# Kernel optimization log

Hardware: AMD Instinct MI355X
Metric: run time of the kernel (lower is better)

Reference implementation:

```python
import jax, jax.numpy as jnp
import numpy as np

VIEW_NUM = 360
CHAN_NUM = 512
BATCH = 2
IMG = 512


def setup_inputs() -> dict:
    key = jax.random.key(0)
    x = jax.random.normal(key, (BATCH, 1, IMG, IMG), dtype=jnp.float32)
    return {"x": x}


def _bilinear_sample_zeros(img, ix, iy):
    """Bilinear sample img (B,1,H,W) at pixel coords ix, iy (H,W), zeros padding.
    Matches F.grid_sample(mode='bilinear', padding_mode='zeros', align_corners=False)."""
    H, W = img.shape[-2], img.shape[-1]
    x0 = jnp.floor(ix)
    y0 = jnp.floor(iy)
    x1 = x0 + 1.0
    y1 = y0 + 1.0
    wx1 = ix - x0
    wx0 = 1.0 - wx1
    wy1 = iy - y0
    wy0 = 1.0 - wy1

    def gather(yy, xx):
        valid = (xx >= 0) & (xx <= W - 1) & (yy >= 0) & (yy <= H - 1)
        xi = jnp.clip(xx, 0, W - 1).astype(jnp.int32)
        yi = jnp.clip(yy, 0, H - 1).astype(jnp.int32)
        # fancy-index over spatial dims -> (B,1,H,W)
        return img[:, :, yi, xi] * valid.astype(img.dtype)

    return (gather(y0, x0) * (wy0 * wx0)
            + gather(y0, x1) * (wy0 * wx1)
            + gather(y1, x0) * (wy1 * wx0)
            + gather(y1, x1) * (wy1 * wx1))


def _fp(x):
    B, C, H, W = x.shape
    # affine_grid base coords, align_corners=False: (2i+1)/N - 1
    bx = (2.0 * jnp.arange(W, dtype=x.dtype) + 1.0) / W - 1.0
    by = (2.0 * jnp.arange(H, dtype=x.dtype) + 1.0) / H - 1.0
    X = bx[None, :]  # (1,W)
    Y = by[:, None]  # (H,1)
    i = jnp.arange(VIEW_NUM, dtype=x.dtype)
    angles = -jnp.pi * (i + 1.0) / VIEW_NUM - jnp.pi
    cosv = jnp.cos(angles)
    sinv = jnp.sin(angles)

    def per_view(carry, cs):
        c, s = cs
        # theta = [[c,-s,0],[s,c,0]]; grid = base @ theta^T
        gx = c * X - s * Y  # (H,W) normalized sample x
        gy = s * X + c * Y  # (H,W) normalized sample y
        # unnormalize (align_corners=False)
        ix = ((gx + 1.0) * W - 1.0) * 0.5
        iy = ((gy + 1.0) * H - 1.0) * 0.5
        samp = _bilinear_sample_zeros(x, ix, iy)  # (B,1,H,W)
        return carry, jnp.sum(samp, axis=2)  # sum over height -> (B,1,W)

    _, cols = jax.lax.scan(per_view, 0, (cosv, sinv))  # (V,B,1,W)
    sino = jnp.transpose(cols, (1, 2, 3, 0)) * 0.5  # (B,1,chanNum,viewNum)
    return sino


def reference(x):
    return _fp(x)
```

## Files before the change

### kernel.cpp

```cpp
#include <hip/hip_runtime.h>

typedef __fp16 h2 __attribute__((ext_vector_type(2)));

constexpr int VIEWS = 360;
constexpr int IMGSZ = 512;
constexpr int WCHUNK = 64;
constexpr int KH = 64;
constexpr int PITCH = 101;
constexpr int MAXNY = 94;
constexpr int LDSDW = PITCH * MAXNY;
constexpr int PW = 712;
constexpr int PH = 704;
constexpr int PAD = 96;
constexpr int NT = 512;

__global__ __launch_bounds__(256) void pad_kernel(const float* __restrict__ x,
                                                  unsigned* __restrict__ padq) {
    constexpr int PW4 = PW / 4;
    constexpr int total = PH * PW4;
    int idx = blockIdx.x * 256 + threadIdx.x;
    if (idx >= total) return;
    int py = idx / PW4;
    int px4 = idx - py * PW4;
    int gx = px4 * 4 - PAD;
    int gy = py - PAD;
    const float* img0 = x;
    const float* img1 = x + (size_t)IMGSZ * IMGSZ;
    float4 a = make_float4(0.f, 0.f, 0.f, 0.f);
    float4 bq = a;
    if ((unsigned)gy < (unsigned)IMGSZ && (unsigned)gx < (unsigned)IMGSZ) {
        size_t off = (size_t)gy * IMGSZ + gx;
        a  = *(const float4*)(img0 + off);
        bq = *(const float4*)(img1 + off);
    }
    uint4 d;
    d.x = __builtin_bit_cast(unsigned, __builtin_amdgcn_cvt_pkrtz(a.x, bq.x));
    d.y = __builtin_bit_cast(unsigned, __builtin_amdgcn_cvt_pkrtz(a.y, bq.y));
    d.z = __builtin_bit_cast(unsigned, __builtin_amdgcn_cvt_pkrtz(a.z, bq.z));
    d.w = __builtin_bit_cast(unsigned, __builtin_amdgcn_cvt_pkrtz(a.w, bq.w));
    *(uint4*)&padq[(size_t)idx * 4] = d;
}

__global__ __launch_bounds__(NT, 8) void fp_kernel(const unsigned* __restrict__ padq,
                                                   float* __restrict__ out) {
    __shared__ __align__(16) unsigned tileU[LDSDW];

    int blk = blockIdx.x;
    int wc = blk & 7;
    int v = blk >> 3;

    int tid = threadIdx.x;
    int lane = tid & 63;
    int p = tid >> 6;
    int w = wc * WCHUNK + lane;

    double ang = -3.14159265358979323846 * (double)(v + 1) / (double)VIEWS
                 - 3.14159265358979323846;
    float c = (float)cos(ang);
    float s = (float)sin(ang);

    float xw = (float)w + 0.5f - 256.0f;
    float cxw = fmaf(c, xw, 255.5f);
    float sxw = fmaf(s, xw, 255.5f);

    float lo = -1e30f, hi = 1e30f;
    {
        float coef = -s, base = cxw;
        if (fabsf(coef) > 1e-6f) {
            float a = (-1.0f - base) / coef;
            float bq = (512.0f - base) / coef;
            lo = fmaxf(lo, fminf(a, bq));
            hi = fminf(hi, fmaxf(a, bq));
        } else if (!(base > -1.0f && base < 512.0f)) {
            lo = 1e30f; hi = -1e30f;
        }
    }
    {
        float coef = c, base = sxw;
        if (fabsf(coef) > 1e-6f) {
            float a = (-1.0f - base) / coef;
            float bq = (512.0f - base) / coef;
            lo = fmaxf(lo, fminf(a, bq));
            hi = fminf(hi, fmaxf(a, bq));
        } else if (!(base > -1.0f && base < 512.0f)) {
            lo = 1e30f; hi = -1e30f;
        }
    }
    float h0f = fminf(fmaxf(floorf(lo + 255.5f) - 1.0f, 0.0f), 512.0f);
    float h1f = fminf(fmaxf(ceilf(hi + 255.5f) + 1.0f, -1.0f), 511.0f);
    int h0 = (int)h0f;
    int h1 = (int)h1f;

    int bh0 = h0, bh1 = h1;
    #pragma unroll
    for (int m = 1; m < 64; m <<= 1) {
        bh0 = min(bh0, __shfl_xor(bh0, m, 64));
        bh1 = max(bh1, __shfl_xor(bh1, m, 64));
    }

    float xa = (float)(wc * WCHUNK) + 0.5f - 256.0f;
    float xb = xa + 63.0f;

    float acc0 = 0.0f, acc1 = 0.0f;
    float step8x = -8.0f * s;
    float step8y = 8.0f * c;

    for (int hc = bh0; hc <= bh1; hc += KH) {
        int hend = min(hc + KH - 1, bh1);

        float ha = (float)hc - 255.5f;
        float hb = (float)hend - 255.5f;
        float ix00 = c * xa - s * ha, ix01 = c * xa - s * hb;
        float ix10 = c * xb - s * ha, ix11 = c * xb - s * hb;
        float iy00 = s * xa + c * ha, iy01 = s * xa + c * hb;
        float iy10 = s * xb + c * ha, iy11 = s * xb + c * hb;
        float ixmn = fminf(fminf(ix00, ix01), fminf(ix10, ix11)) + 255.5f;
        float iymn = fminf(fminf(iy00, iy01), fminf(iy10, iy11)) + 255.5f;
        float iymx = fmaxf(fmaxf(iy00, iy01), fmaxf(iy10, iy11)) + 255.5f;
        int x_lo = (int)floorf(ixmn) - 1;
        int x_lo4 = x_lo & ~3;
        int y_lo = (int)floorf(iymn) - 1;
        int NY = min((int)floorf(iymx) + 3 - y_lo, MAXNY);
        int total4 = NY * 25;
        int nit = (total4 + NT - 1) >> 9;

        __syncthreads();

        {
            const unsigned* pb = padq + (y_lo + PAD) * PW + (x_lo4 + PAD);
            for (int k = 0; k < nit; ++k) {
                int ic = min((k << 9) + tid, total4 - 1);
                int ry = ic / 25;
                uint4 val = *(const uint4*)(pb + 4 * ic + (PW - 100) * ry);
                int d = (ic << 2) + ry;
                tileU[d]     = val.x;
                tileU[d + 1] = val.y;
                tileU[d + 2] = val.z;
                tileU[d + 3] = val.w;
            }
        }
        __syncthreads();

        float hh0 = (float)(hc + p) - 255.5f;
        float ixr = fmaf(-s, hh0, cxw) - (float)x_lo4;
        float iyr = fmaf(c, hh0, sxw) - (float)y_lo;
        h2 accp0 = (h2)0.0f;
        h2 accp1 = (h2)0.0f;
        int parity = 0;
        #pragma unroll 8
        for (int h = hc + p; h <= hend; h += 8) {
            float tx = truncf(ixr);
            float ty = truncf(iyr);
            float wx1 = ixr - tx;
            float wy1 = iyr - ty;
            h2 wxs = __builtin_amdgcn_cvt_pkrtz(wx1, wx1);
            h2 wys = __builtin_amdgcn_cvt_pkrtz(wy1, wy1);
            unsigned a = (unsigned)fmaf(ty, 404.0f, tx * 4.0f);
            const unsigned* pt = (const unsigned*)((const char*)tileU + a);
            h2 t00 = __builtin_bit_cast(h2, pt[0]);
            h2 t01 = __builtin_bit_cast(h2, pt[1]);
            h2 t10 = __builtin_bit_cast(h2, pt[PITCH]);
            h2 t11 = __builtin_bit_cast(h2, pt[PITCH + 1]);
            h2 r0 = t00 + (t01 - t00) * wxs;
            h2 r1 = t10 + (t11 - t10) * wxs;
            h2 contrib = r0 + (r1 - r0) * wys;
            if (parity) accp1 += contrib; else accp0 += contrib;
            parity ^= 1;
            ixr += step8x;
            iyr += step8y;
        }
        acc0 += (float)accp0.x + (float)accp1.x;
        acc1 += (float)accp0.y + (float)accp1.y;
    }

    __syncthreads();
    tileU[(p << 6) + lane] = __float_as_uint(acc0);
    tileU[512 + (p << 6) + lane] = __float_as_uint(acc1);
    __syncthreads();
    if (p < 2) {
        const unsigned* base = tileU + (p << 9);
        float r = 0.0f;
        #pragma unroll
        for (int q = 0; q < 8; ++q) r += __uint_as_float(base[(q << 6) + lane]);
        size_t o = (size_t)w * VIEWS + v;
        out[o + (size_t)p * IMGSZ * VIEWS] = r * 0.5f;
    }
}

extern "C" void kernel_launch(void* const* d_in, const int* in_sizes, int n_in,
                              void* d_out, int out_size, void* d_ws, size_t ws_size,
                              hipStream_t stream) {
    const float* x = (const float*)d_in[0];
    float* out = (float*)d_out;
    unsigned* padq = (unsigned*)d_ws;

    constexpr int padTotal = PH * (PW / 4);
    pad_kernel<<<(padTotal + 255) / 256, 256, 0, stream>>>(x, padq);

    int nblocks = VIEWS * (IMGSZ / WCHUNK);
    fp_kernel<<<nblocks, NT, 0, stream>>>(padq, out);
}
```

Measured before the change: 171.6 us.

## Double-buffer LDS tiles with async global-to-LDS loads overlapping gather

Result: slower. 178.6 us (+4.1%).

```diff
diff --git a/kernel.cpp b/kernel.cpp
--- a/kernel.cpp
+++ b/kernel.cpp
@@ -5,14 +5,20 @@
 constexpr int VIEWS = 360;
 constexpr int IMGSZ = 512;
 constexpr int WCHUNK = 64;
-constexpr int KH = 64;
-constexpr int PITCH = 101;
-constexpr int MAXNY = 94;
-constexpr int LDSDW = PITCH * MAXNY;
+constexpr int KH = 40;
+constexpr int PITCH = 84;
+constexpr int NXF4 = 21;
+constexpr int MAXNY = 79;
+constexpr int TDW = PITCH * MAXNY;
 constexpr int PW = 712;
 constexpr int PH = 704;
 constexpr int PAD = 96;
 constexpr int NT = 512;
+
+#define ASYNC_CP16(SRC, DST)                                              \
+    __builtin_amdgcn_global_load_lds(                                     \
+        (const __attribute__((address_space(1))) unsigned*)(SRC),         \
+        (__attribute__((address_space(3))) unsigned*)(DST), 16, 0, 0)
 
 __global__ __launch_bounds__(256) void pad_kernel(const float* __restrict__ x,
                                                   unsigned* __restrict__ padq) {
@@ -41,9 +47,10 @@
     *(uint4*)&padq[(size_t)idx * 4] = d;
 }
 
-__global__ __launch_bounds__(NT, 8) void fp_kernel(const unsigned* __restrict__ padq,
+__global__ __launch_bounds__(NT, 4) void fp_kernel(const unsigned* __restrict__ padq,
                                                    float* __restrict__ out) {
-    __shared__ __align__(16) unsigned tileU[LDSDW];
+    __shared__ __align__(16) unsigned bufA[TDW];
+    __shared__ __align__(16) unsigned bufB[TDW];
 
     int blk = blockIdx.x;
     int wc = blk & 7;
@@ -105,80 +112,113 @@
     float step8x = -8.0f * s;
     float step8y = 8.0f * c;
 
-    for (int hc = bh0; hc <= bh1; hc += KH) {
-        int hend = min(hc + KH - 1, bh1);
-
-        float ha = (float)hc - 255.5f;
-        float hb = (float)hend - 255.5f;
-        float ix00 = c * xa - s * ha, ix01 = c * xa - s * hb;
-        float ix10 = c * xb - s * ha, ix11 = c * xb - s * hb;
-        float iy00 = s * xa + c * ha, iy01 = s * xa + c * hb;
-        float iy10 = s * xb + c * ha, iy11 = s * xb + c * hb;
-        float ixmn = fminf(fminf(ix00, ix01), fminf(ix10, ix11)) + 255.5f;
-        float iymn = fminf(fminf(iy00, iy01), fminf(iy10, iy11)) + 255.5f;
-        float iymx = fmaxf(fmaxf(iy00, iy01), fmaxf(iy10, iy11)) + 255.5f;
-        int x_lo = (int)floorf(ixmn) - 1;
-        int x_lo4 = x_lo & ~3;
-        int y_lo = (int)floorf(iymn) - 1;
-        int NY = min((int)floorf(iymx) + 3 - y_lo, MAXNY);
-        int total4 = NY * 25;
-        int nit = (total4 + NT - 1) >> 9;
-
+#define BBOX(HC, X4, YL, T4, NIT)                                           \
+    {                                                                       \
+        int hend_ = min((HC) + KH - 1, bh1);                                \
+        float ha_ = (float)(HC) - 255.5f;                                   \
+        float hb_ = (float)hend_ - 255.5f;                                  \
+        float sha_ = s * ha_, shb_ = s * hb_;                               \
+        float cha_ = c * ha_, chb_ = c * hb_;                               \
+        float cxa_ = c * xa, cxb_ = c * xb;                                 \
+        float sxa_ = s * xa, sxb_ = s * xb;                                 \
+        float ixmn_ = fminf(cxa_, cxb_) - fmaxf(sha_, shb_) + 255.5f;       \
+        float iymn_ = fminf(sxa_, sxb_) + fminf(cha_, chb_) + 255.5f;       \
+        float iymx_ = fmaxf(sxa_, sxb_) + fmaxf(cha_, chb_) + 255.5f;       \
+        X4 = ((int)floorf(ixmn_) - 1) & ~3;                                 \
+        YL = (int)floorf(iymn_) - 1;                                        \
+        int NY_ = min((int)floorf(iymx_) + 3 - (YL), MAXNY);                \
+        T4 = NY_ * NXF4;                                                    \
+        NIT = ((T4) + NT - 1) >> 9;                                         \
+    }
+
+#define STAGE(BUF, X4, YL, T4, NIT)                                         \
+    {                                                                       \
+        const unsigned* pb_ = padq + ((YL) + PAD) * PW + ((X4) + PAD);      \
+        for (int k_ = 0; k_ < (NIT); ++k_) {                                \
+            int i_ = (k_ << 9) + tid;                                       \
+            if (((k_ << 9) + (p << 6) + 63) < (T4)) {                       \
+                int ry_ = (i_ * 6242) >> 17;                      \
+                ASYNC_CP16(pb_ + 4 * i_ + (PW - 4 * NXF4) * ry_,            \
+                           &BUF[i_ << 2]);                                  \
+            } else if (i_ < (T4)) {                                         \
+                int ry_ = (i_ * 6242) >> 17;                                \
+                uint4 val_ = *(const uint4*)(pb_ + 4 * i_ +                 \
+                                             (PW - 4 * NXF4) * ry_);        \
+                *(uint4*)&BUF[i_ << 2] = val_;                              \
+            }                                                               \
+        }                                                                   \
+    }
+
+#define GATHER(BUF, HC, X4, YL)                                             \
+    {                                                                       \
+        int hend_ = min((HC) + KH - 1, bh1);                                \
+        float hh0_ = (float)((HC) + p) - 255.5f;                            \
+        float ixr_ = fmaf(-s, hh0_, cxw) - (float)(X4);                     \
+        float iyr_ = fmaf(c, hh0_, sxw) - (float)(YL);                      \
+        h2 a0_ = (h2)0.0f, a1_ = (h2)0.0f;                                  \
+        int par_ = 0;                                                       \
+        _Pragma("unroll 5")                                                 \
+        for (int h_ = (HC) + p; h_ <= hend_; h_ += 8) {                     \
+            float tx_ = truncf(ixr_);                                       \
+            float ty_ = truncf(iyr_);                                       \
+            float wx_ = ixr_ - tx_;                                         \
+            float wy_ = iyr_ - ty_;                                         \
+            h2 wxs_ = __builtin_amdgcn_cvt_pkrtz(wx_, wx_);                 \
+            h2 wys_ = __builtin_amdgcn_cvt_pkrtz(wy_, wy_);                 \
+            unsigned a_ = (unsigned)fmaf(ty_, 336.0f, tx_ * 4.0f);          \
+            const unsigned* pt_ =                                           \
+                (const unsigned*)((const char*)BUF + a_);                   \
+            h2 t00_ = __builtin_bit_cast(h2, pt_[0]);                       \
+            h2 t01_ = __builtin_bit_cast(h2, pt_[1]);                       \
+            h2 t10_ = __builtin_bit_cast(h2, pt_[PITCH]);                   \
+            h2 t11_ = __builtin_bit_cast(h2, pt_[PITCH + 1]);               \
+            h2 r0_ = t00_ + (t01_ - t00_) * wxs_;                           \
+            h2 r1_ = t10_ + (t11_ - t10_) * wxs_;                           \
+            h2 ct_ = r0_ + (r1_ - r0_) * wys_;                              \
+            if (par_) a1_ += ct_; else a0_ += ct_;                          \
+            par_ ^= 1;                                                      \
+            ixr_ += step8x;                                                 \
+            iyr_ += step8y;                                                 \
+        }                                                                   \
+        acc0 += (float)a0_.x + (float)a1_.x;                                \
+        acc1 += (float)a0_.y + (float)a1_.y;                                \
+    }
+
+    if (bh0 <= bh1) {
+        int x4_0, yl_0, t4_0, nit_0;
+        int x4_1, yl_1, t4_1, nit_1;
+
+        BBOX(bh0, x4_0, yl_0, t4_0, nit_0);
+        STAGE(bufA, x4_0, yl_0, t4_0, nit_0);
         __syncthreads();
 
-        {
-            const unsigned* pb = padq + (y_lo + PAD) * PW + (x_lo4 + PAD);
-            for (int k = 0; k < nit; ++k) {
-                int ic = min((k << 9) + tid, total4 - 1);
-                int ry = ic / 25;
-                uint4 val = *(const uint4*)(pb + 4 * ic + (PW - 100) * ry);
-                int d = (ic << 2) + ry;
-                tileU[d]     = val.x;
-                tileU[d + 1] = val.y;
-                tileU[d + 2] = val.z;
-                tileU[d + 3] = val.w;
+        for (int hc = bh0; hc <= bh1; hc += 2 * KH) {
+            int hc1 = hc + KH;
+            if (hc1 <= bh1) {
+                BBOX(hc1, x4_1, yl_1, t4_1, nit_1);
+                STAGE(bufB, x4_1, yl_1, t4_1, nit_1);
+            }
+            GATHER(bufA, hc, x4_0, yl_0);
+            __syncthreads();
+
+            if (hc1 <= bh1) {
+                int hc2 = hc + 2 * KH;
+                if (hc2 <= bh1) {
+                    BBOX(hc2, x4_0, yl_0, t4_0, nit_0);
+                    STAGE(bufA, x4_0, yl_0, t4_0, nit_0);
+                }
+                GATHER(bufB, hc1, x4_1, yl_1);
+                __syncthreads();
             }
         }
-        __syncthreads();
-
-        float hh0 = (float)(hc + p) - 255.5f;
-        float ixr = fmaf(-s, hh0, cxw) - (float)x_lo4;
-        float iyr = fmaf(c, hh0, sxw) - (float)y_lo;
-        h2 accp0 = (h2)0.0f;
-        h2 accp1 = (h2)0.0f;
-        int parity = 0;
-        #pragma unroll 8
-        for (int h = hc + p; h <= hend; h += 8) {
-            float tx = truncf(ixr);
-            float ty = truncf(iyr);
-            float wx1 = ixr - tx;
-            float wy1 = iyr - ty;
-            h2 wxs = __builtin_amdgcn_cvt_pkrtz(wx1, wx1);
-            h2 wys = __builtin_amdgcn_cvt_pkrtz(wy1, wy1);
-            unsigned a = (unsigned)fmaf(ty, 404.0f, tx * 4.0f);
-            const unsigned* pt = (const unsigned*)((const char*)tileU + a);
-            h2 t00 = __builtin_bit_cast(h2, pt[0]);
-            h2 t01 = __builtin_bit_cast(h2, pt[1]);
-            h2 t10 = __builtin_bit_cast(h2, pt[PITCH]);
-            h2 t11 = __builtin_bit_cast(h2, pt[PITCH + 1]);
-            h2 r0 = t00 + (t01 - t00) * wxs;
-            h2 r1 = t10 + (t11 - t10) * wxs;
-            h2 contrib = r0 + (r1 - r0) * wys;
-            if (parity) accp1 += contrib; else accp0 += contrib;
-            parity ^= 1;
-            ixr += step8x;
-            iyr += step8y;
-        }
-        acc0 += (float)accp0.x + (float)accp1.x;
-        acc1 += (float)accp0.y + (float)accp1.y;
     }
 
     __syncthreads();
-    tileU[(p << 6) + lane] = __float_as_uint(acc0);
-    tileU[512 + (p << 6) + lane] = __float_as_uint(acc1);
+    bufA[(p << 6) + lane] = __float_as_uint(acc0);
+    bufA[512 + (p << 6) + lane] = __float_as_uint(acc1);
     __syncthreads();
     if (p < 2) {
-        const unsigned* base = tileU + (p << 9);
+        const unsigned* base = bufA + (p << 9);
         float r = 0.0f;
         #pragma unroll
         for (int q = 0; q < 8; ++q) r += __uint_as_float(base[(q << 6) + lane]);
```
